# Optimization experiments

Measured on AMD Instinct MI355X. Metric: run time of the kernel, lower is better.

The kernel has to match this reference:

```python
import jax, jax.numpy as jnp
import numpy as np

H = 16        # attention heads
KVH = 4       # kv heads (GQA)
D = 128       # qk head_dim = qk_nope(64) + qk_rope(64)
ROPE = 64     # rotary sub-dim
VCH = 128     # v_channels
HID = 2048    # hidden size
E = 8         # routed experts
K = 2         # top-k
EPS = 1e-6
THETA = 10000.0


def rmsnorm(x, w):
    return x * jax.lax.rsqrt(jnp.mean(x * x, axis=-1, keepdims=True) + EPS) * w


def apply_rope(x, pos):
    # x: [T, h, ROPE]; rotate-half convention on the rope sub-dim
    half = ROPE // 2
    inv_freq = 1.0 / (THETA ** (jnp.arange(half, dtype=jnp.float32) / half))
    ang = pos.astype(jnp.float32)[:, None] * inv_freq          # [T, half]
    cos = jnp.cos(ang)[:, None, :]
    sin = jnp.sin(ang)[:, None, :]
    x1, x2 = x[..., :half], x[..., half:]
    return jnp.concatenate([x1 * cos - x2 * sin, x1 * sin + x2 * cos], axis=-1)


def swiglu(x, w_gate, w_up, w_down):
    return (jax.nn.silu(x @ w_gate) * (x @ w_up)) @ w_down


def setup_inputs() -> dict:
    key = jax.random.key(0)
    ks = jax.random.split(key, 16)
    T = 2048
    sc = 0.02
    n = lambda k, s: jax.random.normal(k, s, dtype=jnp.float32) * sc
    return {
        "x": jax.random.normal(ks[0], (T, HID), dtype=jnp.float32),
        "positions": jnp.arange(T, dtype=jnp.int32),
        "ln1_w": jnp.ones((HID,), jnp.float32),
        "qkv_w": n(ks[1], (HID, H * D + KVH * D + KVH * VCH)),
        "qkv_b": n(ks[2], (H * D + KVH * D + KVH * VCH,)),
        "k_ln_w": jnp.ones((D,), jnp.float32),
        "o_w": n(ks[3], (H * VCH, HID)),
        "ln2_w": jnp.ones((HID,), jnp.float32),
        "router_w": n(ks[4], (HID, E)),
        "w1": n(ks[5], (E, HID, 512)),
        "w2": n(ks[6], (E, 512, HID)),
        "w3": n(ks[7], (E, HID, 512)),
        "sw1": n(ks[8], (HID, 1024)),
        "sw2": n(ks[9], (1024, HID)),
        "sw3": n(ks[10], (HID, 1024)),
    }


def reference(x, positions, ln1_w, qkv_w, qkv_b, k_ln_w, o_w, ln2_w,
              router_w, w1, w2, w3, sw1, sw2, sw3):
    T = x.shape[0]
    # --- attention block ---
    h = rmsnorm(x, ln1_w)
    qkv = h @ qkv_w + qkv_b
    q = qkv[:, : H * D].reshape(T, H, D)
    k = qkv[:, H * D : H * D + KVH * D].reshape(T, KVH, D)
    v = qkv[:, H * D + KVH * D :].reshape(T, KVH, VCH)
    k = rmsnorm(k, k_ln_w)  # per-head k_layernorm over head_dim
    # rope applied to the trailing qk_rope_dim of q/k
    q = jnp.concatenate([q[..., : D - ROPE], apply_rope(q[..., D - ROPE :], positions)], -1)
    k = jnp.concatenate([k[..., : D - ROPE], apply_rope(k[..., D - ROPE :], positions)], -1)
    rep = H // KVH
    kf = jnp.repeat(k, rep, axis=1)   # [T, H, D]
    vf = jnp.repeat(v, rep, axis=1)   # [T, H, VCH]
    scale = D ** -0.5
    scores = jnp.einsum("qhd,khd->hqk", q, kf) * scale
    causal = jnp.tril(jnp.ones((T, T), dtype=bool))
    scores = jnp.where(causal[None], scores, jnp.float32(-1e30))
    p = jax.nn.softmax(scores, axis=-1)
    attn = jnp.einsum("hqk,khv->qhv", p, vf).reshape(T, H * VCH)
    x = x + attn @ o_w
    # --- MoE block: shared expert + top-k routed experts ---
    h2 = rmsnorm(x, ln2_w)
    probs = jax.nn.softmax(h2 @ router_w, axis=-1)            # [T, E]
    topw, topi = jax.lax.top_k(probs, K)
    topw = topw / jnp.sum(topw, axis=-1, keepdims=True)        # renormalize top-k
    combine = jnp.sum(jax.nn.one_hot(topi, E, dtype=h2.dtype) * topw[..., None], axis=1)  # [T, E]
    moe = swiglu(h2, sw1, sw3, sw2)                            # shared expert
    for e in range(E):  # small fixed expert count
        moe = moe + combine[:, e : e + 1] * swiglu(h2, w1[e], w3[e], w2[e])
    return x + moe
```

## Files before the change

### kernel.cpp

```cpp
#include <hip/hip_runtime.h>


typedef _Float16 half_t;
typedef _Float16 half8 __attribute__((ext_vector_type(8)));
typedef float    f32x4 __attribute__((ext_vector_type(4)));
typedef float    floatx4 __attribute__((ext_vector_type(4)));

#define T_TOK 2048
#define HIDN  2048
#define NH    16
#define NKVH  4
#define HD    128
#define QKV_N 3072
#define NEXP  8

#define MFMA16(a,b,c) __builtin_amdgcn_mfma_f32_16x16x32_f16(a,b,c,0,0,0)

__device__ __forceinline__ void gload_lds16(const half_t* g, half_t* l) {
    __builtin_amdgcn_global_load_lds(
        (const __attribute__((address_space(1))) void*)g,
        (__attribute__((address_space(3))) void*)l, 16, 0, 0);
}

__global__ __launch_bounds__(256)
void rmsnorm_split_k(const float* __restrict__ x, const float* __restrict__ w,
                     half_t* __restrict__ hi, half_t* __restrict__ lo)
{
    const int row = blockIdx.x, tid = threadIdx.x;
    const float* xr = x + (size_t)row * HIDN;
    floatx4 v0 = *(const floatx4*)(xr + tid * 8);
    floatx4 v1 = *(const floatx4*)(xr + tid * 8 + 4);
    float ss = v0[0]*v0[0] + v0[1]*v0[1] + v0[2]*v0[2] + v0[3]*v0[3]
             + v1[0]*v1[0] + v1[1]*v1[1] + v1[2]*v1[2] + v1[3]*v1[3];
    for (int o = 32; o; o >>= 1) ss += __shfl_down(ss, o);
    __shared__ float red[4];
    if ((tid & 63) == 0) red[tid >> 6] = ss;
    __syncthreads();
    ss = red[0] + red[1] + red[2] + red[3];
    float rs = rsqrtf(ss * (1.0f / HIDN) + 1e-6f);
    floatx4 w0 = *(const floatx4*)(w + tid * 8);
    floatx4 w1 = *(const floatx4*)(w + tid * 8 + 4);
    float vv[8] = { v0[0]*w0[0], v0[1]*w0[1], v0[2]*w0[2], v0[3]*w0[3],
                    v1[0]*w1[0], v1[1]*w1[1], v1[2]*w1[2], v1[3]*w1[3] };
    half8 hv, lv;
#pragma unroll
    for (int j = 0; j < 8; ++j) {
        float o = vv[j] * rs;
        half_t h = (half_t)o;
        hv[j] = h;
        lv[j] = (half_t)((o - (float)h) * 1024.0f);
    }
    *(half8*)(hi + (size_t)row * HIDN + tid * 8) = hv;
    if (lo) *(half8*)(lo + (size_t)row * HIDN + tid * 8) = lv;
}

__global__ __launch_bounds__(256)
void transpose_split2(const float* __restrict__ src, half_t* __restrict__ dh,
                      half_t* __restrict__ dl, int sstride, int dstride)
{
    __shared__ float tile[32][36];
    const int n0 = blockIdx.x * 32, k0 = blockIdx.y * 32;
    const int tid = threadIdx.x;
    {
        int r = tid >> 3, c = (tid & 7) * 4;
        *(floatx4*)&tile[r][c] =
            *(const floatx4*)(src + (size_t)(k0 + r) * sstride + n0 + c);
    }
    __syncthreads();
    int n = tid & 31, g = tid >> 5, gg = g & 3;
    half8 hv;
    if (g < 4) {
#pragma unroll
        for (int j = 0; j < 8; ++j) hv[j] = (half_t)tile[gg * 8 + j][n];
        *(half8*)(dh + (size_t)(n0 + n) * dstride + k0 + gg * 8) = hv;
    } else {
#pragma unroll
        for (int j = 0; j < 8; ++j) {
            float v = tile[gg * 8 + j][n];
            half_t h = (half_t)v;
            hv[j] = (half_t)((v - (float)h) * 1024.0f);
        }
        *(half8*)(dl + (size_t)(n0 + n) * dstride + k0 + gg * 8) = hv;
    }
}

__global__ __launch_bounds__(256)
void w13_transpose(const float* __restrict__ sw1, const float* __restrict__ w1,
                   const float* __restrict__ sw3, const float* __restrict__ w3,
                   half_t* __restrict__ dst)
{
    __shared__ float tile[32][68];
    const int n0 = blockIdx.x * 64, k0 = blockIdx.y * 32;
    const int tid = threadIdx.x;
    const float* base;
    int stride;
    if (n0 < 1024)      { base = sw1 + n0; stride = 1024; }
    else if (n0 < 5120) { int e = (n0 - 1024) >> 9;
                          base = w1 + (size_t)e * HIDN * 512 + ((n0 - 1024) & 511);
                          stride = 512; }
    else if (n0 < 6144) { base = sw3 + (n0 - 5120); stride = 1024; }
    else                { int e = (n0 - 6144) >> 9;
                          base = w3 + (size_t)e * HIDN * 512 + ((n0 - 6144) & 511);
                          stride = 512; }
    {
        int r = tid >> 3, c = (tid & 7) * 4;
        const float* s = base + (size_t)(k0 + r) * stride;
        *(floatx4*)&tile[r][c]      = *(const floatx4*)(s + c);
        *(floatx4*)&tile[r][c + 32] = *(const floatx4*)(s + c + 32);
    }
    __syncthreads();
    int n = tid & 63, g = tid >> 6;
    half8 hv;
#pragma unroll
    for (int j = 0; j < 8; ++j) hv[j] = (half_t)tile[g * 8 + j][n];
    *(half8*)(dst + (size_t)(n0 + n) * HIDN + k0 + g * 8) = hv;
}

__global__ __launch_bounds__(256)
void w2_transpose(const float* __restrict__ sw2, const float* __restrict__ w2,
                  half_t* __restrict__ dst)
{
    __shared__ float tile[32][68];
    const int n0 = blockIdx.x * 64, k0 = blockIdx.y * 32;
    const int tid = threadIdx.x;
    {
        int r = tid >> 3, c = (tid & 7) * 4;
        int k = k0 + r;
        const float* s;
        if (k < 1024) s = sw2 + (size_t)k * HIDN + n0;
        else {
            int e = (k - 1024) >> 9, kk = (k - 1024) & 511;
            s = w2 + ((size_t)e * 512 + kk) * HIDN + n0;
        }
        *(floatx4*)&tile[r][c]      = *(const floatx4*)(s + c);
        *(floatx4*)&tile[r][c + 32] = *(const floatx4*)(s + c + 32);
    }
    __syncthreads();
    int n = tid & 63, g = tid >> 6;
    half8 hv;
#pragma unroll
    for (int j = 0; j < 8; ++j) hv[j] = (half_t)tile[g * 8 + j][n];
    *(half8*)(dst + (size_t)(n0 + n) * 5120 + k0 + g * 8) = hv;
}

template<bool SPLIT, int BM>
__global__ __launch_bounds__(256, 2)
void gemm_f16(const half_t* __restrict__ Ah, const half_t* __restrict__ Al,
              const half_t* __restrict__ Bth, const half_t* __restrict__ Btl,
              const float* __restrict__ bias, const float* __restrict__ res,
              float* __restrict__ Cf, half_t* __restrict__ Ch,
              int M, int N, int K)
{
    constexpr int NBUF = SPLIT ? 2 : 1;
    constexpr int MR = BM / 32;
    __shared__ half_t As[NBUF][BM * 32];
    __shared__ half_t Bs[NBUF][128 * 32];
    const int tid = threadIdx.x, lane = tid & 63, wid = tid >> 6;
    const int l15 = lane & 15, l4 = lane >> 4;
    const int row0 = blockIdx.y * BM, col0 = blockIdx.x * 128;
    const int wr = (wid >> 1) * (BM / 2), wc = (wid & 1) * 64;
    f32x4 accM[MR][4] = {}, accC[MR][4] = {};
    const int lrw = lane >> 2, lcl = (lane & 3) * 8;

    for (int k0 = 0; k0 < K; k0 += 32) {
        __syncthreads();
#pragma unroll
        for (int j = 0; j < BM / 64; ++j) {
            const int r = wid * (BM / 4) + j * 16;
            const size_t ga = (size_t)(row0 + r + lrw) * K + k0 + lcl;
            gload_lds16(Ah + ga, &As[0][r * 32]);
            if constexpr (SPLIT) gload_lds16(Al + ga, &As[1][r * 32]);
        }
#pragma unroll
        for (int j = 0; j < 2; ++j) {
            const int r = wid * 32 + j * 16;
            const size_t gb = (size_t)(col0 + r + lrw) * K + k0 + lcl;
            gload_lds16(Bth + gb, &Bs[0][r * 32]);
            if constexpr (SPLIT) gload_lds16(Btl + gb, &Bs[1][r * 32]);
        }
        __syncthreads();
        half8 ah[MR], al[MR], bh[4], bl[4];
#pragma unroll
        for (int m = 0; m < MR; ++m) {
            int off = (wr + m * 16 + l15) * 32 + l4 * 8;
            ah[m] = *(const half8*)&As[0][off];
            if constexpr (SPLIT) al[m] = *(const half8*)&As[1][off];
        }
#pragma unroll
        for (int n = 0; n < 4; ++n) {
            int off = (wc + n * 16 + l15) * 32 + l4 * 8;
            bh[n] = *(const half8*)&Bs[0][off];
            if constexpr (SPLIT) bl[n] = *(const half8*)&Bs[1][off];
        }
#pragma unroll
        for (int m = 0; m < MR; ++m)
#pragma unroll
            for (int n = 0; n < 4; ++n) {
                accM[m][n] = MFMA16(ah[m], bh[n], accM[m][n]);
                if constexpr (SPLIT) {
                    accC[m][n] = MFMA16(ah[m], bl[n], accC[m][n]);
                    accC[m][n] = MFMA16(al[m], bh[n], accC[m][n]);
                }
            }
    }
#pragma unroll
    for (int m = 0; m < MR; ++m) {
#pragma unroll
        for (int n = 0; n < 4; ++n) {
            int gr0 = row0 + wr + m * 16 + l4 * 4;
            int gc  = col0 + wc + n * 16 + l15;
            float b = bias ? bias[gc] : 0.0f;
#pragma unroll
            for (int i = 0; i < 4; ++i) {
                float v = accM[m][n][i];
                if constexpr (SPLIT) v += accC[m][n][i] * (1.0f / 1024.0f);
                v += b;
                size_t idx = (size_t)(gr0 + i) * N + gc;
                if (res) v += res[idx];
                if (Cf) Cf[idx] = v;
                if (Ch) Ch[idx] = (half_t)v;
            }
        }
    }
}

__global__ __launch_bounds__(256)
void qkv_prep(const float* __restrict__ qkv, const int* __restrict__ pos,
              const float* __restrict__ klnw,
              half_t* __restrict__ qh, half_t* __restrict__ ql,
              half_t* __restrict__ kh, half_t* __restrict__ kl)
{
    const int t = blockIdx.x, tid = threadIdx.x, lane = tid & 63, wid = tid >> 6;
    const float* row = qkv + (size_t)t * QKV_N;
    __shared__ float cs[32], sn[32];
    if (tid < 32) {
        double freq = exp((double)tid * -0.28782313662425572);
        double ang = (double)pos[t] * freq;
        const double twopi = 6.283185307179586476925286766559;
        ang -= twopi * floor(ang * (1.0 / twopi));
        float a = (float)ang;
        cs[tid] = cosf(a);
        sn[tid] = sinf(a);
    }
    __syncthreads();

    const float qscale = 0.08838834764831845f;
    {
        const int hh = tid >> 4, d0 = (tid & 15) * 8;
        const float* qrow = row + hh * HD;
        float outv[8];
        if (d0 < 64) {
#pragma unroll
            for (int j = 0; j < 8; ++j) outv[j] = qrow[d0 + j];
        } else if (d0 < 96) {
            int j0 = d0 - 64;
#pragma unroll
            for (int j = 0; j < 8; ++j) {
                int jj = j0 + j;
                outv[j] = qrow[64 + jj] * cs[jj] - qrow[96 + jj] * sn[jj];
            }
        } else {
            int j0 = d0 - 96;
#pragma unroll
            for (int j = 0; j < 8; ++j) {
                int jj = j0 + j;
                outv[j] = qrow[64 + jj] * sn[jj] + qrow[96 + jj] * cs[jj];
            }
        }
        half8 hv, lv;
#pragma unroll
        for (int j = 0; j < 8; ++j) {
            float o = outv[j] * qscale;
            half_t h = (half_t)o;
            hv[j] = h;
            lv[j] = (half_t)((o - (float)h) * 1024.0f);
        }
        size_t base = (size_t)t * (NH * HD) + hh * HD + d0;
        *(half8*)(qh + base) = hv;
        *(half8*)(ql + base) = lv;
    }
    {
        const float* krow = row + NH * HD + wid * HD;
        float a0 = krow[lane], a1 = krow[64 + lane];
        float ss = a0 * a0 + a1 * a1;
        for (int o = 32; o; o >>= 1) ss += __shfl_down(ss, o);
        ss = __shfl(ss, 0);
        float rs = rsqrtf(ss * (1.0f / HD) + 1e-6f);
        float n0 = a0 * rs * klnw[lane];
        float n1 = a1 * rs * klnw[64 + lane];
        float other = __shfl_xor(n1, 32);
        int j = lane & 31;
        float o1 = (lane < 32) ? (n1 * cs[j] - other * sn[j])
                               : (other * sn[j] + n1 * cs[j]);
        size_t base = (size_t)t * (NKVH * HD) + wid * HD;
        half_t h;
        h = (half_t)n0; kh[base + lane] = h;
        kl[base + lane] = (half_t)((n0 - (float)h) * 1024.0f);
        h = (half_t)o1; kh[base + 64 + lane] = h;
        kl[base + 64 + lane] = (half_t)((o1 - (float)h) * 1024.0f);
    }
}

__global__ __launch_bounds__(256, 2)
void attn_kernel(const half_t* __restrict__ qh, const half_t* __restrict__ ql,
                 const half_t* __restrict__ kh, const half_t* __restrict__ kl,
                 const half_t* __restrict__ vth, const half_t* __restrict__ vtl,
                 half_t* __restrict__ oh, half_t* __restrict__ ol)
{
    const int bid = blockIdx.y * 32 + blockIdx.x;
    int qblk, h;
    if (bid < 256) { qblk = 31 - (bid & 31); h = bid >> 5; }
    else           { qblk = (bid - 256) & 31; h = 8 + ((bid - 256) >> 5); }
    const int kvh = h >> 2;
    const int tid = threadIdx.x, lane = tid & 63, wid = tid >> 6;
    const int q0 = qblk * 64 + wid * 16;
    const int l15 = lane & 15, l4 = lane >> 4;

    __shared__ half_t Ksh[32][136], Ksl[32][136];
    __shared__ half_t Vsh[128][40], Vsl[128][40];
    __shared__ half_t Ph[4][16][40], Pl[4][16][40];

    half8 qfh[4], qfl[4];
    {
        const size_t qb = (size_t)(q0 + l15) * (NH * HD) + h * HD + l4 * 8;
#pragma unroll
        for (int c = 0; c < 4; ++c) {
            qfh[c] = *(const half8*)(qh + qb + c * 32);
            qfl[c] = *(const half8*)(ql + qb + c * 32);
        }
    }

    f32x4 om[8] = {}, oc[8] = {};
    float mrow[4] = { -1e30f, -1e30f, -1e30f, -1e30f };
    float lrow[4] = {};

    const int kr = tid >> 4, kc = (tid & 15) * 8;
    const int vd = tid >> 2, vc = (tid & 3) * 8;
    uint4 rk0h, rk1h, rk0l, rk1l, rv0h, rv1h, rv0l, rv1l;

    const int kvend = qblk * 64 + 64;

#define LOAD_TILE(KV0)                                                        \
    do {                                                                      \
        size_t sk0 = (size_t)((KV0) + kr) * (NKVH * HD) + kvh * HD + kc;      \
        size_t sk1 = sk0 + (size_t)16 * (NKVH * HD);                          \
        rk0h = *(const uint4*)(kh + sk0);  rk0l = *(const uint4*)(kl + sk0);  \
        rk1h = *(const uint4*)(kh + sk1);  rk1l = *(const uint4*)(kl + sk1);  \
        size_t sv0 = (size_t)(kvh * HD + vd) * T_TOK + (KV0) + vc;            \
        size_t sv1 = sv0 + (size_t)64 * T_TOK;                                \
        rv0h = *(const uint4*)(vth + sv0); rv0l = *(const uint4*)(vtl + sv0); \
        rv1h = *(const uint4*)(vth + sv1); rv1l = *(const uint4*)(vtl + sv1); \
    } while (0)

    LOAD_TILE(0);
    for (int kv0 = 0; kv0 < kvend; kv0 += 32) {
        *(uint4*)&Ksh[kr][kc]      = rk0h;  *(uint4*)&Ksl[kr][kc]      = rk0l;
        *(uint4*)&Ksh[kr + 16][kc] = rk1h;  *(uint4*)&Ksl[kr + 16][kc] = rk1l;
        *(uint4*)&Vsh[vd][vc]      = rv0h;  *(uint4*)&Vsl[vd][vc]      = rv0l;
        *(uint4*)&Vsh[vd + 64][vc] = rv1h;  *(uint4*)&Vsl[vd + 64][vc] = rv1l;
        __syncthreads();
        if (kv0 + 32 < kvend) LOAD_TILE(kv0 + 32);

        f32x4 sf[2];
#pragma unroll
        for (int t2 = 0; t2 < 2; ++t2) {
            f32x4 s = {}, sc = {};
#pragma unroll
            for (int c = 0; c < 4; ++c) {
                half8 bh = *(const half8*)&Ksh[t2 * 16 + l15][c * 32 + l4 * 8];
                half8 bl = *(const half8*)&Ksl[t2 * 16 + l15][c * 32 + l4 * 8];
                s  = MFMA16(qfh[c], bh, s);
                sc = MFMA16(qfh[c], bl, sc);
                sc = MFMA16(qfl[c], bh, sc);
            }
            sf[t2] = s + sc * (1.0f / 1024.0f);
        }

        float pmax[4];
#pragma unroll
        for (int i = 0; i < 4; ++i) {
            const int qg = q0 + l4 * 4 + i;
#pragma unroll
            for (int t2 = 0; t2 < 2; ++t2) {
                int kvg = kv0 + t2 * 16 + l15;
                if (kvg > qg) sf[t2][i] = -1e30f;
            }
            float mx = fmaxf(sf[0][i], sf[1][i]);
#pragma unroll
            for (int o = 1; o < 16; o <<= 1) mx = fmaxf(mx, __shfl_xor(mx, o));
            pmax[i] = mx;
        }
        float dm = fmaxf(fmaxf(pmax[0] - mrow[0], pmax[1] - mrow[1]),
                         fmaxf(pmax[2] - mrow[2], pmax[3] - mrow[3]));
        if (__any(dm > 6.0f)) {
#pragma unroll
            for (int i = 0; i < 4; ++i) {
                float mnew = fmaxf(mrow[i], pmax[i]);
                float resc = expf(mrow[i] - mnew);
                lrow[i] *= resc;
#pragma unroll
                for (int c8 = 0; c8 < 8; ++c8) {
                    om[c8][i] *= resc; oc[c8][i] *= resc;
                }
                mrow[i] = mnew;
            }
        }
#pragma unroll
        for (int i = 0; i < 4; ++i) {
            float p0 = expf(sf[0][i] - mrow[i]);
            float p1 = expf(sf[1][i] - mrow[i]);
            lrow[i] += p0 + p1;
            half_t hh;
            hh = (half_t)p0;
            Ph[wid][l4 * 4 + i][l15] = hh;
            Pl[wid][l4 * 4 + i][l15] = (half_t)((p0 - (float)hh) * 1024.0f);
            hh = (half_t)p1;
            Ph[wid][l4 * 4 + i][16 + l15] = hh;
            Pl[wid][l4 * 4 + i][16 + l15] = (half_t)((p1 - (float)hh) * 1024.0f);
        }

        half8 pah = *(const half8*)&Ph[wid][l15][l4 * 8];
        half8 pal = *(const half8*)&Pl[wid][l15][l4 * 8];
#pragma unroll
        for (int c8 = 0; c8 < 8; ++c8) {
            half8 vh = *(const half8*)&Vsh[c8 * 16 + l15][l4 * 8];
            half8 vl = *(const half8*)&Vsl[c8 * 16 + l15][l4 * 8];
            om[c8] = MFMA16(pah, vh, om[c8]);
            oc[c8] = MFMA16(pah, vl, oc[c8]);
            oc[c8] = MFMA16(pal, vh, oc[c8]);
        }
        __syncthreads();
    }
#undef LOAD_TILE

#pragma unroll
    for (int i = 0; i < 4; ++i)
#pragma unroll
        for (int o = 1; o < 16; o <<= 1) lrow[i] += __shfl_xor(lrow[i], o);

#pragma unroll
    for (int c8 = 0; c8 < 8; ++c8) {
#pragma unroll
        for (int i = 0; i < 4; ++i) {
            float v = (om[c8][i] + oc[c8][i] * (1.0f / 1024.0f)) / lrow[i];
            size_t idx = (size_t)(q0 + l4 * 4 + i) * (NH * HD) + h * HD + c8 * 16 + l15;
            half_t hh = (half_t)v;
            oh[idx] = hh;
            ol[idx] = (half_t)((v - (float)hh) * 1024.0f);
        }
    }
}

__global__ __launch_bounds__(256)
void router_kernel(const float* __restrict__ x2, const float* __restrict__ ln2w,
                   const float* __restrict__ rw, float* __restrict__ combine)
{
    const int t = blockIdx.x, tid = threadIdx.x;
    const float* xr = x2 + (size_t)t * HIDN;
    float vals[8];
    float ss = 0.0f;
#pragma unroll
    for (int i = 0; i < 8; ++i) {
        vals[i] = xr[tid + i * 256];
        ss += vals[i] * vals[i];
    }
    for (int o = 32; o; o >>= 1) ss += __shfl_down(ss, o);
    __shared__ float red[4];
    if ((tid & 63) == 0) red[tid >> 6] = ss;
    __syncthreads();
    ss = red[0] + red[1] + red[2] + red[3];
    float rs = rsqrtf(ss * (1.0f / HIDN) + 1e-6f);

    float acc[NEXP] = {};
#pragma unroll
    for (int i = 0; i < 8; ++i) {
        int c = tid + i * 256;
        float hv = vals[i] * rs * ln2w[c];
        const float* wr = rw + (size_t)c * NEXP;
#pragma unroll
        for (int e = 0; e < NEXP; ++e) acc[e] += hv * wr[e];
    }
#pragma unroll
    for (int e = 0; e < NEXP; ++e)
        for (int o = 32; o; o >>= 1) acc[e] += __shfl_down(acc[e], o);
    __shared__ float red8[4][NEXP];
    if ((tid & 63) == 0)
#pragma unroll
        for (int e = 0; e < NEXP; ++e) red8[tid >> 6][e] = acc[e];
    __syncthreads();
    if (tid == 0) {
        float lg[NEXP];
#pragma unroll
        for (int e = 0; e < NEXP; ++e)
            lg[e] = red8[0][e] + red8[1][e] + red8[2][e] + red8[3][e];
        int i1 = 0;
        for (int e = 1; e < NEXP; ++e) if (lg[e] > lg[i1]) i1 = e;
        int i2 = (i1 == 0) ? 1 : 0;
        for (int e = 0; e < NEXP; ++e) if (e != i1 && lg[e] > lg[i2]) i2 = e;
        float mx = lg[i1];
        float p1 = expf(lg[i1] - mx), p2 = expf(lg[i2] - mx);
        float inv = 1.0f / (p1 + p2);
        float* cr = combine + (size_t)t * NEXP;
#pragma unroll
        for (int e = 0; e < NEXP; ++e) cr[e] = 0.0f;
        cr[i1] = p1 * inv;
        cr[i2] = p2 * inv;
    }
}

__global__ __launch_bounds__(256)
void moe_act(const half_t* __restrict__ GU, const float* __restrict__ comb,
             half_t* __restrict__ Abig)
{
    int idx = blockIdx.x * 256 + threadIdx.x;
    int t = idx / 640, c8 = idx % 640;
    int n = c8 * 8;
    half8 g8 = *(const half8*)(GU + (size_t)t * 10240 + n);
    half8 u8 = *(const half8*)(GU + (size_t)t * 10240 + 5120 + n);
    float sc = (n < 1024) ? 1.0f : comb[(size_t)t * NEXP + ((n - 1024) >> 9)];
    half8 o8;
#pragma unroll
    for (int j = 0; j < 8; ++j) {
        float g = (float)g8[j], u = (float)u8[j];
        float s = g / (1.0f + expf(-g));
        o8[j] = (half_t)(s * u * sc);
    }
    *(half8*)(Abig + (size_t)t * 5120 + n) = o8;
}

extern "C" void kernel_launch(void* const* d_in, const int* in_sizes, int n_in,
                              void* d_out, int out_size, void* d_ws, size_t ws_size,
                              hipStream_t stream)
{
    (void)in_sizes; (void)n_in; (void)out_size; (void)ws_size;
    const float* x    = (const float*)d_in[0];
    const int*   pos  = (const int*)  d_in[1];
    const float* ln1w = (const float*)d_in[2];
    const float* qkvw = (const float*)d_in[3];
    const float* qkvb = (const float*)d_in[4];
    const float* klnw = (const float*)d_in[5];
    const float* ow   = (const float*)d_in[6];
    const float* ln2w = (const float*)d_in[7];
    const float* rw   = (const float*)d_in[8];
    const float* w1   = (const float*)d_in[9];
    const float* w2   = (const float*)d_in[10];
    const float* w3   = (const float*)d_in[11];
    const float* sw1  = (const float*)d_in[12];
    const float* sw2  = (const float*)d_in[13];
    const float* sw3  = (const float*)d_in[14];
    float* out = (float*)d_out;

    char* ws = (char*)d_ws;
    const size_t AB = 16842752;
    float*  x2      = (float*)(ws);
    float*  combine = (float*)(ws + 16777216);
    half_t* h_hi    = (half_t*)(ws + AB);
    half_t* h_lo    = (half_t*)(ws + AB + 8388608);
    half_t* qkvwt_h = (half_t*)(ws + AB + 16777216);
    half_t* qkvwt_l = (half_t*)(ws + AB + 29360128);
    float*  qkv     = (float*)(ws + AB + 41943040);
    half_t* q_h     = (half_t*)(ws + AB + 67108864);
    half_t* q_l     = (half_t*)(ws + AB + 75497472);
    half_t* k_h     = (half_t*)(ws + AB + 83886080);
    half_t* k_l     = (half_t*)(ws + AB + 85983232);
    half_t* vt_h    = (half_t*)(ws + AB + 88080384);
    half_t* vt_l    = (half_t*)(ws + AB + 90177536);
    half_t* attn_h  = (half_t*)(ws + AB);
    half_t* attn_l  = (half_t*)(ws + AB + 8388608);
    half_t* owt_h   = (half_t*)(ws + AB + 16777216);
    half_t* owt_l   = (half_t*)(ws + AB + 25165824);
    half_t* h2      = (half_t*)(ws + AB + 33554432);
    half_t* W13t    = (half_t*)(ws + AB + 41943040);
    half_t* GU      = (half_t*)(ws + AB + 83886080);
    half_t* Abig    = (half_t*)(ws + AB);
    half_t* W2t     = (half_t*)(ws + AB + 41943040);

    dim3 b256(256);

    rmsnorm_split_k<<<T_TOK, b256, 0, stream>>>(x, ln1w, h_hi, h_lo);
    transpose_split2<<<dim3(QKV_N / 32, HIDN / 32), b256, 0, stream>>>(
        qkvw, qkvwt_h, qkvwt_l, QKV_N, HIDN);
    gemm_f16<true, 64><<<dim3(QKV_N / 128, T_TOK / 64), b256, 0, stream>>>(
        h_hi, h_lo, qkvwt_h, qkvwt_l, qkvb, nullptr, qkv, nullptr,
        T_TOK, QKV_N, HIDN);
    qkv_prep<<<T_TOK, b256, 0, stream>>>(qkv, pos, klnw, q_h, q_l, k_h, k_l);
    transpose_split2<<<dim3(512 / 32, T_TOK / 32), b256, 0, stream>>>(
        qkv + 2560, vt_h, vt_l, QKV_N, T_TOK);
    transpose_split2<<<dim3(HIDN / 32, HIDN / 32), b256, 0, stream>>>(
        ow, owt_h, owt_l, HIDN, HIDN);
    attn_kernel<<<dim3(32, NH), b256, 0, stream>>>(
        q_h, q_l, k_h, k_l, vt_h, vt_l, attn_h, attn_l);
    gemm_f16<true, 64><<<dim3(HIDN / 128, T_TOK / 64), b256, 0, stream>>>(
        attn_h, attn_l, owt_h, owt_l, nullptr, x, x2, nullptr,
        T_TOK, HIDN, HIDN);
    router_kernel<<<T_TOK, b256, 0, stream>>>(x2, ln2w, rw, combine);
    rmsnorm_split_k<<<T_TOK, b256, 0, stream>>>(x2, ln2w, h2, nullptr);
    w13_transpose<<<dim3(10240 / 64, HIDN / 32), b256, 0, stream>>>(
        sw1, w1, sw3, w3, W13t);
    gemm_f16<false, 128><<<dim3(10240 / 128, T_TOK / 128), b256, 0, stream>>>(
        h2, nullptr, W13t, nullptr, nullptr, nullptr, nullptr, GU,
        T_TOK, 10240, HIDN);
    w2_transpose<<<dim3(HIDN / 64, 5120 / 32), b256, 0, stream>>>(sw2, w2, W2t);
    moe_act<<<(T_TOK * 640) / 256, b256, 0, stream>>>(GU, combine, Abig);
    gemm_f16<false, 64><<<dim3(HIDN / 128, T_TOK / 64), b256, 0, stream>>>(
        Abig, nullptr, W2t, nullptr, nullptr, x2, out, nullptr,
        T_TOK, HIDN, 5120);
}
```

Before: 643.6 us.

## Drop split-precision o_proj GEMM; compute router logits via precomposed o_w·router weights

The o_proj GEMM now runs in plain fp16 instead of the hi/lo split. This removes two of its three MFMA passes and the low-half weight transpose. To keep expert selection accurate, router logits are computed from the split-precision attention output and a precomputed (o_w·diag(ln2w)·router_w) matrix plus x·ln2w·router_w, scaled by the rmsnorm factor of x2. Attention also gets a flat block ordering by descending q-block and s_setprio around the MFMA sections. The change risks reduced accuracy in x2 and the MoE output, and adds a small owu kernel.

```diff
diff --git a/kernel.cpp b/kernel.cpp
--- a/kernel.cpp
+++ b/kernel.cpp
@@ -82,6 +82,27 @@
         }
         *(half8*)(dl + (size_t)(n0 + n) * dstride + k0 + gg * 8) = hv;
     }
+}
+
+__global__ __launch_bounds__(256)
+void transpose_f16(const float* __restrict__ src, half_t* __restrict__ dh,
+                   int sstride, int dstride)
+{
+    __shared__ float tile[32][68];
+    const int n0 = blockIdx.x * 64, k0 = blockIdx.y * 32;
+    const int tid = threadIdx.x;
+    {
+        int r = tid >> 3, c = (tid & 7) * 4;
+        const float* s = src + (size_t)(k0 + r) * sstride + n0;
+        *(floatx4*)&tile[r][c]      = *(const floatx4*)(s + c);
+        *(floatx4*)&tile[r][c + 32] = *(const floatx4*)(s + c + 32);
+    }
+    __syncthreads();
+    int n = tid & 63, g = tid >> 6;
+    half8 hv;
+#pragma unroll
+    for (int j = 0; j < 8; ++j) hv[j] = (half_t)tile[g * 8 + j][n];
+    *(half8*)(dh + (size_t)(n0 + n) * dstride + k0 + g * 8) = hv;
 }
 
 __global__ __launch_bounds__(256)
@@ -141,6 +162,36 @@
 #pragma unroll
     for (int j = 0; j < 8; ++j) hv[j] = (half_t)tile[g * 8 + j][n];
     *(half8*)(dst + (size_t)(n0 + n) * 5120 + k0 + g * 8) = hv;
+}
+
+__global__ __launch_bounds__(256)
+void owu_kernel(const float* __restrict__ ow, const float* __restrict__ ln2w,
+                const float* __restrict__ rw, float* __restrict__ owu)
+{
+    const int k = blockIdx.x * 4 + (threadIdx.x >> 6);
+    const int lane = threadIdx.x & 63;
+    float acc[NEXP] = {};
+    const float* row = ow + (size_t)k * HIDN;
+#pragma unroll
+    for (int j = 0; j < 8; ++j) {
+        int c = j * 256 + lane * 4;
+        floatx4 ov = *(const floatx4*)(row + c);
+        floatx4 lw = *(const floatx4*)(ln2w + c);
+#pragma unroll
+        for (int i = 0; i < 4; ++i) {
+            float s = ov[i] * lw[i];
+            const float* rwc = rw + (size_t)(c + i) * NEXP;
+#pragma unroll
+            for (int e = 0; e < NEXP; ++e) acc[e] += s * rwc[e];
+        }
+    }
+#pragma unroll
+    for (int e = 0; e < NEXP; ++e)
+        for (int o = 32; o; o >>= 1) acc[e] += __shfl_down(acc[e], o);
+    if (lane == 0) {
+#pragma unroll
+        for (int e = 0; e < NEXP; ++e) owu[(size_t)k * NEXP + e] = acc[e];
+    }
 }
 
 template<bool SPLIT, int BM>
@@ -307,10 +358,9 @@
                  const half_t* __restrict__ vth, const half_t* __restrict__ vtl,
                  half_t* __restrict__ oh, half_t* __restrict__ ol)
 {
-    const int bid = blockIdx.y * 32 + blockIdx.x;
-    int qblk, h;
-    if (bid < 256) { qblk = 31 - (bid & 31); h = bid >> 5; }
-    else           { qblk = (bid - 256) & 31; h = 8 + ((bid - 256) >> 5); }
+    const int bid = blockIdx.x;
+    const int qblk = 31 - (bid >> 4);
+    const int h = bid & 15;
     const int kvh = h >> 2;
     const int tid = threadIdx.x, lane = tid & 63, wid = tid >> 6;
     const int q0 = qblk * 64 + wid * 16;
@@ -362,6 +412,7 @@
         if (kv0 + 32 < kvend) LOAD_TILE(kv0 + 32);
 
         f32x4 sf[2];
+        __builtin_amdgcn_s_setprio(1);
 #pragma unroll
         for (int t2 = 0; t2 < 2; ++t2) {
             f32x4 s = {}, sc = {};
@@ -375,6 +426,7 @@
             }
             sf[t2] = s + sc * (1.0f / 1024.0f);
         }
+        __builtin_amdgcn_s_setprio(0);
 
         float pmax[4];
 #pragma unroll
@@ -421,6 +473,7 @@
 
         half8 pah = *(const half8*)&Ph[wid][l15][l4 * 8];
         half8 pal = *(const half8*)&Pl[wid][l15][l4 * 8];
+        __builtin_amdgcn_s_setprio(1);
 #pragma unroll
         for (int c8 = 0; c8 < 8; ++c8) {
             half8 vh = *(const half8*)&Vsh[c8 * 16 + l15][l4 * 8];
@@ -429,6 +482,7 @@
             oc[c8] = MFMA16(pah, vl, oc[c8]);
             oc[c8] = MFMA16(pal, vh, oc[c8]);
         }
+        __builtin_amdgcn_s_setprio(0);
         __syncthreads();
     }
 #undef LOAD_TILE
@@ -452,17 +506,18 @@
 }
 
 __global__ __launch_bounds__(256)
-void router_kernel(const float* __restrict__ x2, const float* __restrict__ ln2w,
-                   const float* __restrict__ rw, float* __restrict__ combine)
+void router_linear(const float* __restrict__ x, const half_t* __restrict__ ah,
+                   const half_t* __restrict__ al, const float* __restrict__ x2,
+                   const float* __restrict__ ln2w, const float* __restrict__ rw,
+                   const float* __restrict__ owu, float* __restrict__ combine)
 {
     const int t = blockIdx.x, tid = threadIdx.x;
-    const float* xr = x2 + (size_t)t * HIDN;
-    float vals[8];
+    const float* xr2 = x2 + (size_t)t * HIDN;
     float ss = 0.0f;
 #pragma unroll
     for (int i = 0; i < 8; ++i) {
-        vals[i] = xr[tid + i * 256];
-        ss += vals[i] * vals[i];
+        float v = xr2[tid + i * 256];
+        ss += v * v;
     }
     for (int o = 32; o; o >>= 1) ss += __shfl_down(ss, o);
     __shared__ float red[4];
@@ -471,14 +526,19 @@
     ss = red[0] + red[1] + red[2] + red[3];
     float rs = rsqrtf(ss * (1.0f / HIDN) + 1e-6f);
 
+    const float* xr = x + (size_t)t * HIDN;
+    const half_t* ar = ah + (size_t)t * HIDN;
+    const half_t* alr = al + (size_t)t * HIDN;
     float acc[NEXP] = {};
 #pragma unroll
     for (int i = 0; i < 8; ++i) {
         int c = tid + i * 256;
-        float hv = vals[i] * rs * ln2w[c];
-        const float* wr = rw + (size_t)c * NEXP;
-#pragma unroll
-        for (int e = 0; e < NEXP; ++e) acc[e] += hv * wr[e];
+        float xv = xr[c] * ln2w[c];
+        float ap = (float)ar[c] + (float)alr[c] * (1.0f / 1024.0f);
+        const float* rwc = rw + (size_t)c * NEXP;
+        const float* owc = owu + (size_t)c * NEXP;
+#pragma unroll
+        for (int e = 0; e < NEXP; ++e) acc[e] += xv * rwc[e] + ap * owc[e];
     }
 #pragma unroll
     for (int e = 0; e < NEXP; ++e)
@@ -492,7 +552,7 @@
         float lg[NEXP];
 #pragma unroll
         for (int e = 0; e < NEXP; ++e)
-            lg[e] = red8[0][e] + red8[1][e] + red8[2][e] + red8[3][e];
+            lg[e] = (red8[0][e] + red8[1][e] + red8[2][e] + red8[3][e]) * rs;
         int i1 = 0;
         for (int e = 1; e < NEXP; ++e) if (lg[e] > lg[i1]) i1 = e;
         int i2 = (i1 == 0) ? 1 : 0;
@@ -567,8 +627,8 @@
     half_t* vt_l    = (half_t*)(ws + AB + 90177536);
     half_t* attn_h  = (half_t*)(ws + AB);
     half_t* attn_l  = (half_t*)(ws + AB + 8388608);
-    half_t* owt_h   = (half_t*)(ws + AB + 16777216);
-    half_t* owt_l   = (half_t*)(ws + AB + 25165824);
+    half_t* owt     = (half_t*)(ws + AB + 16777216);
+    float*  ow_u    = (float*)(ws + AB + 25165824);
     half_t* h2      = (half_t*)(ws + AB + 33554432);
     half_t* W13t    = (half_t*)(ws + AB + 41943040);
     half_t* GU      = (half_t*)(ws + AB + 83886080);
@@ -586,14 +646,16 @@
     qkv_prep<<<T_TOK, b256, 0, stream>>>(qkv, pos, klnw, q_h, q_l, k_h, k_l);
     transpose_split2<<<dim3(512 / 32, T_TOK / 32), b256, 0, stream>>>(
         qkv + 2560, vt_h, vt_l, QKV_N, T_TOK);
-    transpose_split2<<<dim3(HIDN / 32, HIDN / 32), b256, 0, stream>>>(
-        ow, owt_h, owt_l, HIDN, HIDN);
-    attn_kernel<<<dim3(32, NH), b256, 0, stream>>>(
+    transpose_f16<<<dim3(HIDN / 64, HIDN / 32), b256, 0, stream>>>(
+        ow, owt, HIDN, HIDN);
+    owu_kernel<<<512, b256, 0, stream>>>(ow, ln2w, rw, ow_u);
+    attn_kernel<<<512, b256, 0, stream>>>(
         q_h, q_l, k_h, k_l, vt_h, vt_l, attn_h, attn_l);
-    gemm_f16<true, 64><<<dim3(HIDN / 128, T_TOK / 64), b256, 0, stream>>>(
-        attn_h, attn_l, owt_h, owt_l, nullptr, x, x2, nullptr,
+    gemm_f16<false, 64><<<dim3(HIDN / 128, T_TOK / 64), b256, 0, stream>>>(
+        attn_h, nullptr, owt, nullptr, nullptr, x, x2, nullptr,
         T_TOK, HIDN, HIDN);
-    router_kernel<<<T_TOK, b256, 0, stream>>>(x2, ln2w, rw, combine);
+    router_linear<<<T_TOK, b256, 0, stream>>>(
+        x, attn_h, attn_l, x2, ln2w, rw, ow_u, combine);
     rmsnorm_split_k<<<T_TOK, b256, 0, stream>>>(x2, ln2w, h2, nullptr);
     w13_transpose<<<dim3(10240 / 64, HIDN / 32), b256, 0, stream>>>(
         sw1, w1, sw3, w3, W13t);
```

Result: no change. 648.9 us (+0.8%).
